# Kernel tuning notes

Hardware: AMD Instinct MI355X
Metric: run time of the kernel (lower is better)

The kernel has to match this reference:

```python
import jax, jax.numpy as jnp
import numpy as np

BN_EPS = 1e-5

def setup_inputs() -> dict:
    key = jax.random.key(0)
    B, C, T, N = 64, 1, 1024, 512
    weighted_fmri = jax.random.normal(key, (B, C, T, N), dtype=jnp.float32)
    bn_weight = jnp.ones((1,), dtype=jnp.float32)   # BatchNorm2d(1) affine weight
    bn_bias = jnp.zeros((1,), dtype=jnp.float32)    # BatchNorm2d(1) affine bias
    return {"weighted_fmri": weighted_fmri, "bn_weight": bn_weight, "bn_bias": bn_bias}


def reference(weighted_fmri, bn_weight, bn_bias):
    # weighted_fmri: [B, 1, T, N]. Original applies BatchNorm2d(1) per-sample
    # (batch of size 1 in training mode => normalize each sample by its own
    # mean/biased-var over (T, N)), then corrcoef over ROIs (columns).
    x = weighted_fmri
    mean = jnp.mean(x, axis=(1, 2, 3), keepdims=True)           # [B,1,1,1]
    var = jnp.mean((x - mean) ** 2, axis=(1, 2, 3), keepdims=True)  # biased var
    w = bn_weight.reshape(1, -1, 1, 1)
    b = bn_bias.reshape(1, -1, 1, 1)
    y = (x - mean) * jax.lax.rsqrt(var + BN_EPS) * w + b        # [B,1,T,N]

    X = y[:, 0]                                                 # [B,T,N]
    T = X.shape[1]
    # corrcoef(X.T): variables = N ROIs, observations = T timepoints
    Xc = X - jnp.mean(X, axis=1, keepdims=True)                 # center over time
    cov = jnp.einsum("btn,btm->bnm", Xc, Xc) / (T - 1)          # [B,N,N]
    d = jnp.sqrt(jnp.diagonal(cov, axis1=1, axis2=2))           # [B,N]
    corr = cov / (d[:, :, None] * d[:, None, :])
    return jnp.clip(corr, -1.0, 1.0)                            # [B,N,N]
```

## Files before the change

kernel.cpp:

```cpp
#include <hip/hip_runtime.h>

typedef __attribute__((ext_vector_type(8))) short bf16x8;
typedef __attribute__((ext_vector_type(4))) short s16x4;
typedef __attribute__((ext_vector_type(4))) float f32x4;

#define B_ 64
#define T_ 1024
#define N_ 512

__device__ __forceinline__ void async16(const void* g, void* l) {
  __builtin_amdgcn_global_load_lds(
      (const __attribute__((address_space(1))) unsigned int*)g,
      (__attribute__((address_space(3))) unsigned int*)l, 16, 0, 0);
}

__device__ __forceinline__ short f2bf(float f) {
  unsigned u = __builtin_bit_cast(unsigned, f);
  u += 0x7fffu + ((u >> 16) & 1u);
  return (short)(u >> 16);
}
__device__ __forceinline__ float bf2f(short s) {
  return __builtin_bit_cast(float, ((unsigned)(unsigned short)s) << 16);
}

__global__ __launch_bounds__(256, 4) void k_prep(
    const float* __restrict__ X, short* __restrict__ XbT,
    float* __restrict__ amu, float* __restrict__ invd)
{
  __shared__ __align__(16) short tile[64][68];
  const int b   = blockIdx.y;
  const int n0  = blockIdx.x * 64;
  const int tid = threadIdx.x;
  const int nch = tid & 15;
  const int rg  = tid >> 4;

  float s[4] = {0.f,0.f,0.f,0.f}, q[4] = {0.f,0.f,0.f,0.f};

  for (int tt = 0; tt < 16; ++tt) {
    const int t0 = tt * 64;
    #pragma unroll
    for (int i = 0; i < 4; ++i) {
      const int tr = rg + i * 16;
      const float4 v = *(const float4*)&X[((size_t)b*T_ + t0 + tr)*N_ + n0 + nch*4];
      short bb[4];
      bb[0] = f2bf(v.x); bb[1] = f2bf(v.y); bb[2] = f2bf(v.z); bb[3] = f2bf(v.w);
      #pragma unroll
      for (int c = 0; c < 4; ++c) { float f = bf2f(bb[c]); s[c] += f; q[c] += f*f; }
      s16x4 pk = { bb[0], bb[1], bb[2], bb[3] };
      *(s16x4*)&tile[tr][nch*4] = pk;
    }
    __syncthreads();
    #pragma unroll
    for (int i = 0; i < 4; ++i) {
      const int n = rg + i * 16;
      s16x4 o = { tile[nch*4+0][n], tile[nch*4+1][n],
                  tile[nch*4+2][n], tile[nch*4+3][n] };
      *(s16x4*)&XbT[((size_t)b*N_ + n0 + n)*T_ + t0 + nch*4] = o;
    }
    __syncthreads();
  }

  float* fb = (float*)&tile[0][0];
  #pragma unroll
  for (int c = 0; c < 4; ++c) { fb[tid*8 + c] = s[c]; fb[tid*8 + 4 + c] = q[c]; }
  __syncthreads();
  if (tid < 64) {
    const int qc = tid >> 2, c = tid & 3;
    float cs = 0.f, sq = 0.f;
    #pragma unroll
    for (int g = 0; g < 16; ++g) {
      cs += fb[(g*16 + qc)*8 + c];
      sq += fb[(g*16 + qc)*8 + 4 + c];
    }
    const int n = n0 + qc*4 + c;
    amu[b*N_ + n]  = cs * (1.f/32.f);
    invd[b*N_ + n] = rsqrtf(fmaxf(sq - cs*cs*(1.f/1024.f), 1e-20f));
  }
}

__global__ __launch_bounds__(256, 2) void k_gram(
    const short* __restrict__ XbT, const float* __restrict__ amu,
    const float* __restrict__ invd, float* __restrict__ out)
{
  __shared__ __align__(16) short ldsA[2][128][32];
  __shared__ __align__(16) short ldsB[2][128][32];

  const int bid = (blockIdx.x & 7) * 80 + (blockIdx.x >> 3);
  const int b = bid / 10;
  const int t = bid - b * 10;
  const int ip = (t >= 4) + (t >= 7) + (t >= 9);
  const int jp = ip + t - ((ip * (9 - ip)) >> 1);
  const int rowBase = ip * 128, colBase = jp * 128;
  const bool diag = (ip == jp);

  const int tid = threadIdx.x, lane = tid & 63, wave = tid >> 6;
  const int wr = wave >> 1, wc = wave & 1;
  const short* Xb = XbT + (size_t)b * N_ * T_;

  const int r0 = tid >> 2, cl = tid & 3;
  const int cg = cl ^ ((r0 >> 1) & 3);
  const size_t ga0 = (size_t)(rowBase + r0)      * T_ + cg * 8;
  const size_t ga1 = (size_t)(rowBase + r0 + 64) * T_ + cg * 8;
  const size_t gb0 = (size_t)(colBase + r0)      * T_ + cg * 8;
  const size_t gb1 = (size_t)(colBase + r0 + 64) * T_ + cg * 8;

  const int fr = lane & 15, kc = lane >> 4;
  const int swz = (kc ^ ((fr >> 1) & 3)) * 8;

  f32x4 acc[4][4] = {};

  #define STAGE(bufi, kb)                                                    \
    do {                                                                     \
      char* la_ = (char*)&ldsA[bufi][0][0];                                  \
      async16(Xb + ga0 + (kb), la_ + tid * 16);                              \
      async16(Xb + ga1 + (kb), la_ + (tid + 256) * 16);                      \
      if (!diag) {                                                           \
        char* lb_ = (char*)&ldsB[bufi][0][0];                                \
        async16(Xb + gb0 + (kb), lb_ + tid * 16);                            \
        async16(Xb + gb1 + (kb), lb_ + (tid + 256) * 16);                    \
      }                                                                      \
    } while (0)

  STAGE(0, 0);
  __syncthreads();
  int cur = 0;
  #pragma unroll 1
  for (int kt = 0; kt < 32; ++kt) {
    if (kt < 31) STAGE(cur ^ 1, (kt + 1) * 32);
    const short (*A)[32]  = ldsA[cur];
    const short (*Bm)[32] = diag ? ldsA[cur] : ldsB[cur];
    bf16x8 af[4], bfv[4];
    #pragma unroll
    for (int mi = 0; mi < 4; ++mi)
      af[mi] = *(const bf16x8*)&A[wr*64 + mi*16 + fr][swz];
    #pragma unroll
    for (int ni = 0; ni < 4; ++ni)
      bfv[ni] = *(const bf16x8*)&Bm[wc*64 + ni*16 + fr][swz];
    #pragma unroll
    for (int mi = 0; mi < 4; ++mi)
      #pragma unroll
      for (int ni = 0; ni < 4; ++ni)
        acc[mi][ni] = __builtin_amdgcn_mfma_f32_16x16x32_bf16(
            af[mi], bfv[ni], acc[mi][ni], 0, 0, 0);
    __syncthreads();
    cur ^= 1;
  }

  const int jc = colBase + wc * 64 + fr;
  float aj[4], dj[4];
  #pragma unroll
  for (int ni = 0; ni < 4; ++ni) {
    aj[ni] = amu[b*N_ + jc + ni*16];
    dj[ni] = invd[b*N_ + jc + ni*16];
  }
  #pragma unroll
  for (int mi = 0; mi < 4; ++mi) {
    const int ibase = rowBase + wr*64 + mi*16 + kc*4;
    float ai[4], di[4];
    #pragma unroll
    for (int r = 0; r < 4; ++r) {
      ai[r] = amu[b*N_ + ibase + r];
      di[r] = invd[b*N_ + ibase + r];
    }
    #pragma unroll
    for (int ni = 0; ni < 4; ++ni) {
      f32x4 g;
      #pragma unroll
      for (int r = 0; r < 4; ++r) {
        float v = (acc[mi][ni][r] - ai[r]*aj[ni]) * (di[r]*dj[ni]);
        g[r] = fminf(fmaxf(v, -1.f), 1.f);
      }
      const int J = jc + ni*16;
      #pragma unroll
      for (int r = 0; r < 4; ++r)
        out[((size_t)b*N_ + ibase + r)*N_ + J] = g[r];
      if (!diag)
        *(f32x4*)&out[((size_t)b*N_ + J)*N_ + ibase] = g;
    }
  }
}

extern "C" void kernel_launch(void* const* d_in, const int* in_sizes, int n_in,
                              void* d_out, int out_size, void* d_ws, size_t ws_size,
                              hipStream_t stream) {
  const float* X = (const float*)d_in[0];
  float* out = (float*)d_out;

  char* ws = (char*)d_ws;
  short* XbT  = (short*)ws;
  size_t off  = (size_t)B_ * N_ * T_ * sizeof(short);
  float* amu  = (float*)(ws + off);
  float* invd = amu + B_ * N_;

  k_prep<<<dim3(N_/64, B_), 256, 0, stream>>>(X, XbT, amu, invd);
  k_gram<<<dim3(64 * 10), 256, 0, stream>>>(XbT, amu, invd, out);
}
```

Before: 70.07 us.

## Fuse bf16 conversion into Gram kernels and compute stats via MFMA on diagonal tiles

```diff
diff --git a/kernel.cpp b/kernel.cpp
--- a/kernel.cpp
+++ b/kernel.cpp
@@ -1,4 +1,5 @@
 #include <hip/hip_runtime.h>
+#include <hip/hip_bf16.h>
 
 typedef __attribute__((ext_vector_type(8))) short bf16x8;
 typedef __attribute__((ext_vector_type(4))) short s16x4;
@@ -8,140 +9,171 @@
 #define T_ 1024
 #define N_ 512
 
-__device__ __forceinline__ void async16(const void* g, void* l) {
-  __builtin_amdgcn_global_load_lds(
-      (const __attribute__((address_space(1))) unsigned int*)g,
-      (__attribute__((address_space(3))) unsigned int*)l, 16, 0, 0);
-}
-
-__device__ __forceinline__ short f2bf(float f) {
-  unsigned u = __builtin_bit_cast(unsigned, f);
-  u += 0x7fffu + ((u >> 16) & 1u);
-  return (short)(u >> 16);
-}
-__device__ __forceinline__ float bf2f(short s) {
-  return __builtin_bit_cast(float, ((unsigned)(unsigned short)s) << 16);
-}
-
-__global__ __launch_bounds__(256, 4) void k_prep(
-    const float* __restrict__ X, short* __restrict__ XbT,
-    float* __restrict__ amu, float* __restrict__ invd)
+struct Slab { float4 v[4]; };
+
+__device__ __forceinline__ void slab_load(const float* __restrict__ Xb, int kb,
+                                          int pbase, int tid, Slab& s) {
+  const int n = (tid & 31) * 4, k = (tid >> 5) * 4;
+  const float* base = Xb + (size_t)(kb + k) * N_ + pbase + n;
+  #pragma unroll
+  for (int r = 0; r < 4; ++r)
+    s.v[r] = *(const float4*)(base + (size_t)r * N_);
+}
+
+__device__ __forceinline__ void slab_write(short* lds, int tid, const Slab& s) {
+  const int nq = tid & 31, kq = tid >> 5;
+  const int cg = kq >> 1, h = kq & 1;
+  const float* f = (const float*)&s.v[0];
+  #pragma unroll
+  for (int c = 0; c < 4; ++c) {
+    const int row = nq * 4 + c;
+    const int cc = cg ^ ((row >> 1) & 3);
+    s16x4 pk;
+    #pragma unroll
+    for (int r = 0; r < 4; ++r)
+      pk[r] = __builtin_bit_cast(short, __float2bfloat16(f[r * 4 + c]));
+    *(s16x4*)&lds[row * 32 + cc * 8 + h * 4] = pk;
+  }
+}
+
+__device__ __forceinline__ bf16x8 frag(const short* lds, int row, int kc) {
+  return *(const bf16x8*)&lds[row * 32 + ((kc ^ ((row >> 1) & 3)) * 8)];
+}
+
+__global__ __launch_bounds__(256, 2) void k_diag(
+    const float* __restrict__ X, float* __restrict__ amu,
+    float* __restrict__ invd, float* __restrict__ out)
 {
-  __shared__ __align__(16) short tile[64][68];
-  const int b   = blockIdx.y;
-  const int n0  = blockIdx.x * 64;
-  const int tid = threadIdx.x;
-  const int nch = tid & 15;
-  const int rg  = tid >> 4;
-
-  float s[4] = {0.f,0.f,0.f,0.f}, q[4] = {0.f,0.f,0.f,0.f};
-
-  for (int tt = 0; tt < 16; ++tt) {
-    const int t0 = tt * 64;
-    #pragma unroll
-    for (int i = 0; i < 4; ++i) {
-      const int tr = rg + i * 16;
-      const float4 v = *(const float4*)&X[((size_t)b*T_ + t0 + tr)*N_ + n0 + nch*4];
-      short bb[4];
-      bb[0] = f2bf(v.x); bb[1] = f2bf(v.y); bb[2] = f2bf(v.z); bb[3] = f2bf(v.w);
-      #pragma unroll
-      for (int c = 0; c < 4; ++c) { float f = bf2f(bb[c]); s[c] += f; q[c] += f*f; }
-      s16x4 pk = { bb[0], bb[1], bb[2], bb[3] };
-      *(s16x4*)&tile[tr][nch*4] = pk;
-    }
+  __shared__ __align__(16) short lds[2][128 * 32];
+  __shared__ float sAmu[128], sInvd[128];
+  const int p = blockIdx.x, b = blockIdx.y, pbase = p * 128;
+  const int tid = threadIdx.x, lane = tid & 63, wave = tid >> 6;
+  const int wr = wave >> 1, wc = wave & 1;
+  const int fr = lane & 15, kc = lane >> 4;
+  const float* Xb = X + (size_t)b * T_ * N_;
+
+  f32x4 acc[4][4] = {};
+  f32x4 accR[4] = {};
+  const short oneb = (short)0x3F80;
+  const bf16x8 ones = { oneb,oneb,oneb,oneb,oneb,oneb,oneb,oneb };
+
+  #define COMPUTE(BUF)                                                        \
+    do {                                                                      \
+      bf16x8 af[4], bfv[4];                                                   \
+      _Pragma("unroll")                                                       \
+      for (int mi = 0; mi < 4; ++mi) af[mi] = frag(BUF, wr*64 + mi*16 + fr, kc); \
+      _Pragma("unroll")                                                       \
+      for (int ni = 0; ni < 4; ++ni) bfv[ni] = frag(BUF, wc*64 + ni*16 + fr, kc); \
+      _Pragma("unroll")                                                       \
+      for (int mi = 0; mi < 4; ++mi) {                                        \
+        accR[mi] = __builtin_amdgcn_mfma_f32_16x16x32_bf16(af[mi], ones, accR[mi], 0,0,0); \
+        _Pragma("unroll")                                                     \
+        for (int ni = 0; ni < 4; ++ni)                                        \
+          acc[mi][ni] = __builtin_amdgcn_mfma_f32_16x16x32_bf16(af[mi], bfv[ni], acc[mi][ni], 0,0,0); \
+      }                                                                       \
+    } while (0)
+
+  Slab sA, sB;
+  slab_load(Xb, 0,  pbase, tid, sA);
+  slab_load(Xb, 32, pbase, tid, sB);
+  slab_write(lds[0], tid, sA);
+  __syncthreads();
+  #pragma unroll 1
+  for (int kt = 0; kt < 32; kt += 2) {
+    if (kt + 2 < 32) slab_load(Xb, (kt + 2) * 32, pbase, tid, sA);
+    COMPUTE(lds[0]);
+    slab_write(lds[1], tid, sB);
     __syncthreads();
-    #pragma unroll
-    for (int i = 0; i < 4; ++i) {
-      const int n = rg + i * 16;
-      s16x4 o = { tile[nch*4+0][n], tile[nch*4+1][n],
-                  tile[nch*4+2][n], tile[nch*4+3][n] };
-      *(s16x4*)&XbT[((size_t)b*N_ + n0 + n)*T_ + t0 + nch*4] = o;
-    }
+    if (kt + 3 < 32) slab_load(Xb, (kt + 3) * 32, pbase, tid, sB);
+    COMPUTE(lds[1]);
+    if (kt + 2 < 32) slab_write(lds[0], tid, sA);
     __syncthreads();
   }
 
-  float* fb = (float*)&tile[0][0];
-  #pragma unroll
-  for (int c = 0; c < 4; ++c) { fb[tid*8 + c] = s[c]; fb[tid*8 + 4 + c] = q[c]; }
+  if ((wave == 0 || wave == 3) && kc == (fr >> 2)) {
+    const int r = fr & 3;
+    #pragma unroll
+    for (int mi = 0; mi < 4; ++mi) {
+      const int il = wr * 64 + mi * 16 + fr;
+      const float rs  = accR[mi][r];
+      const float sii = acc[mi][mi][r];
+      const float a  = rs * (1.f / 32.f);
+      const float id = rsqrtf(fmaxf(sii - rs * rs * (1.f / 1024.f), 1e-20f));
+      sAmu[il] = a; sInvd[il] = id;
+      amu [b * N_ + pbase + il] = a;
+      invd[b * N_ + pbase + il] = id;
+    }
+  }
   __syncthreads();
-  if (tid < 64) {
-    const int qc = tid >> 2, c = tid & 3;
-    float cs = 0.f, sq = 0.f;
-    #pragma unroll
-    for (int g = 0; g < 16; ++g) {
-      cs += fb[(g*16 + qc)*8 + c];
-      sq += fb[(g*16 + qc)*8 + 4 + c];
-    }
-    const int n = n0 + qc*4 + c;
-    amu[b*N_ + n]  = cs * (1.f/32.f);
-    invd[b*N_ + n] = rsqrtf(fmaxf(sq - cs*cs*(1.f/1024.f), 1e-20f));
-  }
-}
-
-__global__ __launch_bounds__(256, 2) void k_gram(
-    const short* __restrict__ XbT, const float* __restrict__ amu,
+
+  const int jl = wc * 64 + fr;
+  float aj[4], dj[4];
+  #pragma unroll
+  for (int ni = 0; ni < 4; ++ni) { aj[ni] = sAmu[jl + ni*16]; dj[ni] = sInvd[jl + ni*16]; }
+  #pragma unroll
+  for (int mi = 0; mi < 4; ++mi) {
+    const int il = wr * 64 + mi * 16 + kc * 4;
+    float ai[4], di[4];
+    #pragma unroll
+    for (int r = 0; r < 4; ++r) { ai[r] = sAmu[il + r]; di[r] = sInvd[il + r]; }
+    #pragma unroll
+    for (int ni = 0; ni < 4; ++ni) {
+      #pragma unroll
+      for (int r = 0; r < 4; ++r) {
+        float v = (acc[mi][ni][r] - ai[r] * aj[ni]) * (di[r] * dj[ni]);
+        v = fminf(fmaxf(v, -1.f), 1.f);
+        out[((size_t)b * N_ + pbase + il + r) * N_ + pbase + jl + ni * 16] = v;
+      }
+    }
+  }
+  #undef COMPUTE
+}
+
+__global__ __launch_bounds__(256, 2) void k_off(
+    const float* __restrict__ X, const float* __restrict__ amu,
     const float* __restrict__ invd, float* __restrict__ out)
 {
-  __shared__ __align__(16) short ldsA[2][128][32];
-  __shared__ __align__(16) short ldsB[2][128][32];
-
-  const int bid = (blockIdx.x & 7) * 80 + (blockIdx.x >> 3);
-  const int b = bid / 10;
-  const int t = bid - b * 10;
-  const int ip = (t >= 4) + (t >= 7) + (t >= 9);
-  const int jp = ip + t - ((ip * (9 - ip)) >> 1);
+  __shared__ __align__(16) short ldsA[2][128 * 32];
+  __shared__ __align__(16) short ldsB[2][128 * 32];
+  const int bid = (blockIdx.x & 7) * 48 + (blockIdx.x >> 3);
+  const int b = bid / 6, t = bid - b * 6;
+  const int ip = (t >= 3) + (t >= 5);
+  const int jp = (ip == 0) ? t + 1 : (ip == 1 ? t - 1 : 3);
   const int rowBase = ip * 128, colBase = jp * 128;
-  const bool diag = (ip == jp);
-
   const int tid = threadIdx.x, lane = tid & 63, wave = tid >> 6;
   const int wr = wave >> 1, wc = wave & 1;
-  const short* Xb = XbT + (size_t)b * N_ * T_;
-
-  const int r0 = tid >> 2, cl = tid & 3;
-  const int cg = cl ^ ((r0 >> 1) & 3);
-  const size_t ga0 = (size_t)(rowBase + r0)      * T_ + cg * 8;
-  const size_t ga1 = (size_t)(rowBase + r0 + 64) * T_ + cg * 8;
-  const size_t gb0 = (size_t)(colBase + r0)      * T_ + cg * 8;
-  const size_t gb1 = (size_t)(colBase + r0 + 64) * T_ + cg * 8;
-
   const int fr = lane & 15, kc = lane >> 4;
-  const int swz = (kc ^ ((fr >> 1) & 3)) * 8;
+  const float* Xb = X + (size_t)b * T_ * N_;
 
   f32x4 acc[4][4] = {};
 
-  #define STAGE(bufi, kb)                                                    \
-    do {                                                                     \
-      char* la_ = (char*)&ldsA[bufi][0][0];                                  \
-      async16(Xb + ga0 + (kb), la_ + tid * 16);                              \
-      async16(Xb + ga1 + (kb), la_ + (tid + 256) * 16);                      \
-      if (!diag) {                                                           \
-        char* lb_ = (char*)&ldsB[bufi][0][0];                                \
-        async16(Xb + gb0 + (kb), lb_ + tid * 16);                            \
-        async16(Xb + gb1 + (kb), lb_ + (tid + 256) * 16);                    \
-      }                                                                      \
-    } while (0)
-
-  STAGE(0, 0);
+  Slab a0, b0;
+  slab_load(Xb, 0, rowBase, tid, a0);
+  slab_load(Xb, 0, colBase, tid, b0);
+  slab_write(ldsA[0], tid, a0);
+  slab_write(ldsB[0], tid, b0);
   __syncthreads();
   int cur = 0;
   #pragma unroll 1
   for (int kt = 0; kt < 32; ++kt) {
-    if (kt < 31) STAGE(cur ^ 1, (kt + 1) * 32);
-    const short (*A)[32]  = ldsA[cur];
-    const short (*Bm)[32] = diag ? ldsA[cur] : ldsB[cur];
+    if (kt < 31) {
+      slab_load(Xb, (kt + 1) * 32, rowBase, tid, a0);
+      slab_load(Xb, (kt + 1) * 32, colBase, tid, b0);
+    }
     bf16x8 af[4], bfv[4];
     #pragma unroll
+    for (int mi = 0; mi < 4; ++mi) af[mi] = frag(ldsA[cur], wr*64 + mi*16 + fr, kc);
+    #pragma unroll
+    for (int ni = 0; ni < 4; ++ni) bfv[ni] = frag(ldsB[cur], wc*64 + ni*16 + fr, kc);
+    #pragma unroll
     for (int mi = 0; mi < 4; ++mi)
-      af[mi] = *(const bf16x8*)&A[wr*64 + mi*16 + fr][swz];
-    #pragma unroll
-    for (int ni = 0; ni < 4; ++ni)
-      bfv[ni] = *(const bf16x8*)&Bm[wc*64 + ni*16 + fr][swz];
-    #pragma unroll
-    for (int mi = 0; mi < 4; ++mi)
       #pragma unroll
       for (int ni = 0; ni < 4; ++ni)
-        acc[mi][ni] = __builtin_amdgcn_mfma_f32_16x16x32_bf16(
-            af[mi], bfv[ni], acc[mi][ni], 0, 0, 0);
+        acc[mi][ni] = __builtin_amdgcn_mfma_f32_16x16x32_bf16(af[mi], bfv[ni], acc[mi][ni], 0,0,0);
+    if (kt < 31) {
+      slab_write(ldsA[cur ^ 1], tid, a0);
+      slab_write(ldsB[cur ^ 1], tid, b0);
+    }
     __syncthreads();
     cur ^= 1;
   }
@@ -150,32 +182,31 @@
   float aj[4], dj[4];
   #pragma unroll
   for (int ni = 0; ni < 4; ++ni) {
-    aj[ni] = amu[b*N_ + jc + ni*16];
-    dj[ni] = invd[b*N_ + jc + ni*16];
+    aj[ni] = amu [b * N_ + jc + ni * 16];
+    dj[ni] = invd[b * N_ + jc + ni * 16];
   }
   #pragma unroll
   for (int mi = 0; mi < 4; ++mi) {
-    const int ibase = rowBase + wr*64 + mi*16 + kc*4;
+    const int ibase = rowBase + wr * 64 + mi * 16 + kc * 4;
     float ai[4], di[4];
     #pragma unroll
     for (int r = 0; r < 4; ++r) {
-      ai[r] = amu[b*N_ + ibase + r];
-      di[r] = invd[b*N_ + ibase + r];
+      ai[r] = amu [b * N_ + ibase + r];
+      di[r] = invd[b * N_ + ibase + r];
     }
     #pragma unroll
     for (int ni = 0; ni < 4; ++ni) {
       f32x4 g;
       #pragma unroll
       for (int r = 0; r < 4; ++r) {
-        float v = (acc[mi][ni][r] - ai[r]*aj[ni]) * (di[r]*dj[ni]);
+        float v = (acc[mi][ni][r] - ai[r] * aj[ni]) * (di[r] * dj[ni]);
         g[r] = fminf(fmaxf(v, -1.f), 1.f);
       }
-      const int J = jc + ni*16;
+      const int J = jc + ni * 16;
       #pragma unroll
       for (int r = 0; r < 4; ++r)
-        out[((size_t)b*N_ + ibase + r)*N_ + J] = g[r];
-      if (!diag)
-        *(f32x4*)&out[((size_t)b*N_ + J)*N_ + ibase] = g;
+        out[((size_t)b * N_ + ibase + r) * N_ + J] = g[r];
+      *(f32x4*)&out[((size_t)b * N_ + J) * N_ + ibase] = g;
     }
   }
 }
@@ -186,12 +217,9 @@
   const float* X = (const float*)d_in[0];
   float* out = (float*)d_out;
 
-  char* ws = (char*)d_ws;
-  short* XbT  = (short*)ws;
-  size_t off  = (size_t)B_ * N_ * T_ * sizeof(short);
-  float* amu  = (float*)(ws + off);
+  float* amu  = (float*)d_ws;
   float* invd = amu + B_ * N_;
 
-  k_prep<<<dim3(N_/64, B_), 256, 0, stream>>>(X, XbT, amu, invd);
-  k_gram<<<dim3(64 * 10), 256, 0, stream>>>(XbT, amu, invd, out);
-}
+  k_diag<<<dim3(4, B_), 256, 0, stream>>>(X, amu, invd, out);
+  k_off<<<dim3(8 * 48), 256, 0, stream>>>(X, amu, invd, out);
+}
```

After: 76.21 us. 1.09x slower.

## Triple-buffer gram kernel LDS pipeline with explicit vmcnt waits and diag specialization

Applied to the files above, without the earlier changes.

```diff
diff --git a/kernel.cpp b/kernel.cpp
--- a/kernel.cpp
+++ b/kernel.cpp
@@ -1,4 +1,5 @@
 #include <hip/hip_runtime.h>
+#include <hip/hip_bf16.h>
 
 typedef __attribute__((ext_vector_type(8))) short bf16x8;
 typedef __attribute__((ext_vector_type(4))) short s16x4;
@@ -7,6 +8,10 @@
 #define B_ 64
 #define T_ 1024
 #define N_ 512
+
+#define FENCE() asm volatile("" ::: "memory")
+#define VMWAIT(N) asm volatile("s_waitcnt vmcnt(" #N ")" ::: "memory")
+#define BAR() __builtin_amdgcn_s_barrier()
 
 __device__ __forceinline__ void async16(const void* g, void* l) {
   __builtin_amdgcn_global_load_lds(
@@ -15,9 +20,7 @@
 }
 
 __device__ __forceinline__ short f2bf(float f) {
-  unsigned u = __builtin_bit_cast(unsigned, f);
-  u += 0x7fffu + ((u >> 16) & 1u);
-  return (short)(u >> 16);
+  return __builtin_bit_cast(short, __float2bfloat16(f));
 }
 __device__ __forceinline__ float bf2f(short s) {
   return __builtin_bit_cast(float, ((unsigned)(unsigned short)s) << 16);
@@ -78,12 +81,78 @@
   }
 }
 
-__global__ __launch_bounds__(256, 2) void k_gram(
+__device__ __forceinline__ void compute_step(
+    const short* A, const short* Bm, int aoff, int boff, int swz,
+    f32x4 (&acc)[4][4])
+{
+  bf16x8 af[4], bfv[4];
+  #pragma unroll
+  for (int mi = 0; mi < 4; ++mi) af[mi] = *(const bf16x8*)&A[aoff + mi*512 + swz];
+  #pragma unroll
+  for (int ni = 0; ni < 4; ++ni) bfv[ni] = *(const bf16x8*)&Bm[boff + ni*512 + swz];
+  #pragma unroll
+  for (int mi = 0; mi < 4; ++mi)
+    #pragma unroll
+    for (int ni = 0; ni < 4; ++ni)
+      acc[mi][ni] = __builtin_amdgcn_mfma_f32_16x16x32_bf16(
+          af[mi], bfv[ni], acc[mi][ni], 0, 0, 0);
+}
+
+template<bool DIAG>
+__device__ __forceinline__ void gram_main(
+    const short* __restrict__ Xb,
+    size_t ga0, size_t ga1, size_t gb0, size_t gb1,
+    short (*ldsA)[4096], short (*ldsB)[4096],
+    int tid, int aoff, int boff, int swz, f32x4 (&acc)[4][4])
+{
+  auto stg = [&](int bi, int kb) {
+    char* la = (char*)ldsA[bi];
+    async16(Xb + ga0 + kb, la + tid*16);
+    async16(Xb + ga1 + kb, la + (tid+256)*16);
+    if (!DIAG) {
+      char* lb = (char*)ldsB[bi];
+      async16(Xb + gb0 + kb, lb + tid*16);
+      async16(Xb + gb1 + kb, lb + (tid+256)*16);
+    }
+  };
+  auto cmp = [&](int bi) {
+    compute_step(ldsA[bi], DIAG ? ldsA[bi] : ldsB[bi], aoff, boff, swz, acc);
+  };
+
+  stg(0, 0); stg(1, 32);
+  #pragma unroll 1
+  for (int it = 0; it < 10; ++it) {
+    stg(2, (3*it + 2) * 32);
+    if (DIAG) { VMWAIT(4); } else { VMWAIT(8); }
+    BAR(); FENCE();
+    cmp(0);
+    FENCE(); BAR();
+    stg(0, (3*it + 3) * 32);
+    if (DIAG) { VMWAIT(4); } else { VMWAIT(8); }
+    BAR(); FENCE();
+    cmp(1);
+    FENCE(); BAR();
+    stg(1, (3*it + 4) * 32);
+    if (DIAG) { VMWAIT(4); } else { VMWAIT(8); }
+    BAR(); FENCE();
+    cmp(2);
+    FENCE(); BAR();
+  }
+  if (DIAG) { VMWAIT(2); } else { VMWAIT(4); }
+  BAR(); FENCE();
+  cmp(0);
+  FENCE(); BAR();
+  VMWAIT(0);
+  BAR(); FENCE();
+  cmp(1);
+}
+
+__global__ __launch_bounds__(256, 3) void k_gram(
     const short* __restrict__ XbT, const float* __restrict__ amu,
     const float* __restrict__ invd, float* __restrict__ out)
 {
-  __shared__ __align__(16) short ldsA[2][128][32];
-  __shared__ __align__(16) short ldsB[2][128][32];
+  __shared__ __align__(16) short ldsA[3][4096];
+  __shared__ __align__(16) short ldsB[3][4096];
 
   const int bid = (blockIdx.x & 7) * 80 + (blockIdx.x >> 3);
   const int b = bid / 10;
@@ -105,52 +174,19 @@
   const size_t gb1 = (size_t)(colBase + r0 + 64) * T_ + cg * 8;
 
   const int fr = lane & 15, kc = lane >> 4;
-  const int swz = (kc ^ ((fr >> 1) & 3)) * 8;
+  const int swz  = (kc ^ ((fr >> 1) & 3)) * 8;
+  const int aoff = (wr * 64 + fr) * 32;
+  const int boff = (wc * 64 + fr) * 32;
 
   f32x4 acc[4][4] = {};
-
-  #define STAGE(bufi, kb)                                                    \
-    do {                                                                     \
-      char* la_ = (char*)&ldsA[bufi][0][0];                                  \
-      async16(Xb + ga0 + (kb), la_ + tid * 16);                              \
-      async16(Xb + ga1 + (kb), la_ + (tid + 256) * 16);                      \
-      if (!diag) {                                                           \
-        char* lb_ = (char*)&ldsB[bufi][0][0];                                \
-        async16(Xb + gb0 + (kb), lb_ + tid * 16);                            \
-        async16(Xb + gb1 + (kb), lb_ + (tid + 256) * 16);                    \
-      }                                                                      \
-    } while (0)
-
-  STAGE(0, 0);
-  __syncthreads();
-  int cur = 0;
-  #pragma unroll 1
-  for (int kt = 0; kt < 32; ++kt) {
-    if (kt < 31) STAGE(cur ^ 1, (kt + 1) * 32);
-    const short (*A)[32]  = ldsA[cur];
-    const short (*Bm)[32] = diag ? ldsA[cur] : ldsB[cur];
-    bf16x8 af[4], bfv[4];
-    #pragma unroll
-    for (int mi = 0; mi < 4; ++mi)
-      af[mi] = *(const bf16x8*)&A[wr*64 + mi*16 + fr][swz];
-    #pragma unroll
-    for (int ni = 0; ni < 4; ++ni)
-      bfv[ni] = *(const bf16x8*)&Bm[wc*64 + ni*16 + fr][swz];
-    #pragma unroll
-    for (int mi = 0; mi < 4; ++mi)
-      #pragma unroll
-      for (int ni = 0; ni < 4; ++ni)
-        acc[mi][ni] = __builtin_amdgcn_mfma_f32_16x16x32_bf16(
-            af[mi], bfv[ni], acc[mi][ni], 0, 0, 0);
-    __syncthreads();
-    cur ^= 1;
-  }
+  if (diag) gram_main<true >(Xb, ga0, ga1, gb0, gb1, ldsA, ldsB, tid, aoff, boff, swz, acc);
+  else      gram_main<false>(Xb, ga0, ga1, gb0, gb1, ldsA, ldsB, tid, aoff, boff, swz, acc);
 
   const int jc = colBase + wc * 64 + fr;
   float aj[4], dj[4];
   #pragma unroll
   for (int ni = 0; ni < 4; ++ni) {
-    aj[ni] = amu[b*N_ + jc + ni*16];
+    aj[ni] = amu [b*N_ + jc + ni*16];
     dj[ni] = invd[b*N_ + jc + ni*16];
   }
   #pragma unroll
@@ -159,7 +195,7 @@
     float ai[4], di[4];
     #pragma unroll
     for (int r = 0; r < 4; ++r) {
-      ai[r] = amu[b*N_ + ibase + r];
+      ai[r] = amu [b*N_ + ibase + r];
       di[r] = invd[b*N_ + ibase + r];
     }
     #pragma unroll
@@ -170,7 +206,7 @@
         float v = (acc[mi][ni][r] - ai[r]*aj[ni]) * (di[r]*dj[ni]);
         g[r] = fminf(fmaxf(v, -1.f), 1.f);
       }
-      const int J = jc + ni*16;
+      const int J = jc + ni * 16;
       #pragma unroll
       for (int r = 0; r < 4; ++r)
         out[((size_t)b*N_ + ibase + r)*N_ + J] = g[r];
```

Result: faster. 68.24 us (-2.6%).

## Fuse bf16 transpose-prep into gram kernel, computing column stats in-block

Applied to the files above, without the earlier changes.

```diff
diff --git a/kernel.cpp b/kernel.cpp
--- a/kernel.cpp
+++ b/kernel.cpp
@@ -1,4 +1,5 @@
 #include <hip/hip_runtime.h>
+#include <hip/hip_bf16.h>
 
 typedef __attribute__((ext_vector_type(8))) short bf16x8;
 typedef __attribute__((ext_vector_type(4))) short s16x4;
@@ -8,82 +9,66 @@
 #define T_ 1024
 #define N_ 512
 
-__device__ __forceinline__ void async16(const void* g, void* l) {
-  __builtin_amdgcn_global_load_lds(
-      (const __attribute__((address_space(1))) unsigned int*)g,
-      (__attribute__((address_space(3))) unsigned int*)l, 16, 0, 0);
-}
-
 __device__ __forceinline__ short f2bf(float f) {
-  unsigned u = __builtin_bit_cast(unsigned, f);
-  u += 0x7fffu + ((u >> 16) & 1u);
-  return (short)(u >> 16);
+  return __builtin_bit_cast(short, __float2bfloat16(f));
 }
 __device__ __forceinline__ float bf2f(short s) {
   return __builtin_bit_cast(float, ((unsigned)(unsigned short)s) << 16);
 }
 
-__global__ __launch_bounds__(256, 4) void k_prep(
-    const float* __restrict__ X, short* __restrict__ XbT,
-    float* __restrict__ amu, float* __restrict__ invd)
-{
-  __shared__ __align__(16) short tile[64][68];
-  const int b   = blockIdx.y;
-  const int n0  = blockIdx.x * 64;
-  const int tid = threadIdx.x;
-  const int nch = tid & 15;
-  const int rg  = tid >> 4;
+struct Slab { float4 v[4]; };
 
-  float s[4] = {0.f,0.f,0.f,0.f}, q[4] = {0.f,0.f,0.f,0.f};
+__device__ __forceinline__ void slab_load(const float* __restrict__ Xb, int kb,
+                                          int pbase, int tid, Slab& s) {
+  const int n = (tid & 31) * 4, k = (tid >> 5) * 4;
+  const float* base = Xb + (size_t)(kb + k) * N_ + pbase + n;
+  #pragma unroll
+  for (int r = 0; r < 4; ++r)
+    s.v[r] = *(const float4*)(base + (size_t)r * N_);
+}
 
-  for (int tt = 0; tt < 16; ++tt) {
-    const int t0 = tt * 64;
+__device__ __forceinline__ void slab_write(short* lds, int tid, const Slab& s,
+                                           float (&st)[4], float (&qt)[4]) {
+  const int nq = tid & 31, kq = tid >> 5;
+  const int cg = kq >> 1, h = kq & 1;
+  const float* f = (const float*)&s.v[0];
+  #pragma unroll
+  for (int c = 0; c < 4; ++c) {
+    const int row = nq * 4 + c;
+    const int cc = cg ^ ((row >> 1) & 3);
+    s16x4 pk;
     #pragma unroll
-    for (int i = 0; i < 4; ++i) {
-      const int tr = rg + i * 16;
-      const float4 v = *(const float4*)&X[((size_t)b*T_ + t0 + tr)*N_ + n0 + nch*4];
-      short bb[4];
-      bb[0] = f2bf(v.x); bb[1] = f2bf(v.y); bb[2] = f2bf(v.z); bb[3] = f2bf(v.w);
-      #pragma unroll
-      for (int c = 0; c < 4; ++c) { float f = bf2f(bb[c]); s[c] += f; q[c] += f*f; }
-      s16x4 pk = { bb[0], bb[1], bb[2], bb[3] };
-      *(s16x4*)&tile[tr][nch*4] = pk;
+    for (int r = 0; r < 4; ++r) {
+      pk[r] = f2bf(f[r * 4 + c]);
+      const float fv = bf2f(pk[r]);
+      st[c] += fv; qt[c] += fv * fv;
     }
-    __syncthreads();
-    #pragma unroll
-    for (int i = 0; i < 4; ++i) {
-      const int n = rg + i * 16;
-      s16x4 o = { tile[nch*4+0][n], tile[nch*4+1][n],
-                  tile[nch*4+2][n], tile[nch*4+3][n] };
-      *(s16x4*)&XbT[((size_t)b*N_ + n0 + n)*T_ + t0 + nch*4] = o;
-    }
-    __syncthreads();
-  }
-
-  float* fb = (float*)&tile[0][0];
-  #pragma unroll
-  for (int c = 0; c < 4; ++c) { fb[tid*8 + c] = s[c]; fb[tid*8 + 4 + c] = q[c]; }
-  __syncthreads();
-  if (tid < 64) {
-    const int qc = tid >> 2, c = tid & 3;
-    float cs = 0.f, sq = 0.f;
-    #pragma unroll
-    for (int g = 0; g < 16; ++g) {
-      cs += fb[(g*16 + qc)*8 + c];
-      sq += fb[(g*16 + qc)*8 + 4 + c];
-    }
-    const int n = n0 + qc*4 + c;
-    amu[b*N_ + n]  = cs * (1.f/32.f);
-    invd[b*N_ + n] = rsqrtf(fmaxf(sq - cs*cs*(1.f/1024.f), 1e-20f));
+    *(s16x4*)&lds[row * 32 + cc * 8 + h * 4] = pk;
   }
 }
 
-__global__ __launch_bounds__(256, 2) void k_gram(
-    const short* __restrict__ XbT, const float* __restrict__ amu,
-    const float* __restrict__ invd, float* __restrict__ out)
+__device__ __forceinline__ void compute_step(
+    const short* A, const short* Bm, int aoff, int boff, int swz,
+    f32x4 (&acc)[4][4])
 {
-  __shared__ __align__(16) short ldsA[2][128][32];
-  __shared__ __align__(16) short ldsB[2][128][32];
+  bf16x8 af[4], bfv[4];
+  #pragma unroll
+  for (int mi = 0; mi < 4; ++mi) af[mi] = *(const bf16x8*)&A[aoff + mi*512 + swz];
+  #pragma unroll
+  for (int ni = 0; ni < 4; ++ni) bfv[ni] = *(const bf16x8*)&Bm[boff + ni*512 + swz];
+  #pragma unroll
+  for (int mi = 0; mi < 4; ++mi)
+    #pragma unroll
+    for (int ni = 0; ni < 4; ++ni)
+      acc[mi][ni] = __builtin_amdgcn_mfma_f32_16x16x32_bf16(
+          af[mi], bfv[ni], acc[mi][ni], 0, 0, 0);
+}
+
+__global__ __launch_bounds__(256, 3) void k_fused(
+    const float* __restrict__ X, float* __restrict__ out)
+{
+  __shared__ __align__(16) short lds[2][2][4096];
+  __shared__ float sMu[256], sId[256];
 
   const int bid = (blockIdx.x & 7) * 80 + (blockIdx.x >> 3);
   const int b = bid / 10;
@@ -95,87 +80,93 @@
 
   const int tid = threadIdx.x, lane = tid & 63, wave = tid >> 6;
   const int wr = wave >> 1, wc = wave & 1;
-  const short* Xb = XbT + (size_t)b * N_ * T_;
+  const int fr = lane & 15, kc = lane >> 4;
+  const int swz  = (kc ^ ((fr >> 1) & 3)) * 8;
+  const int aoff = (wr * 64 + fr) * 32;
+  const int boff = (wc * 64 + fr) * 32;
+  const float* Xb = X + (size_t)b * T_ * N_;
 
-  const int r0 = tid >> 2, cl = tid & 3;
-  const int cg = cl ^ ((r0 >> 1) & 3);
-  const size_t ga0 = (size_t)(rowBase + r0)      * T_ + cg * 8;
-  const size_t ga1 = (size_t)(rowBase + r0 + 64) * T_ + cg * 8;
-  const size_t gb0 = (size_t)(colBase + r0)      * T_ + cg * 8;
-  const size_t gb1 = (size_t)(colBase + r0 + 64) * T_ + cg * 8;
-
-  const int fr = lane & 15, kc = lane >> 4;
-  const int swz = (kc ^ ((fr >> 1) & 3)) * 8;
-
+  float sA[4] = {0,0,0,0}, qA[4] = {0,0,0,0};
+  float sB[4] = {0,0,0,0}, qB[4] = {0,0,0,0};
   f32x4 acc[4][4] = {};
 
-  #define STAGE(bufi, kb)                                                    \
-    do {                                                                     \
-      char* la_ = (char*)&ldsA[bufi][0][0];                                  \
-      async16(Xb + ga0 + (kb), la_ + tid * 16);                              \
-      async16(Xb + ga1 + (kb), la_ + (tid + 256) * 16);                      \
-      if (!diag) {                                                           \
-        char* lb_ = (char*)&ldsB[bufi][0][0];                                \
-        async16(Xb + gb0 + (kb), lb_ + tid * 16);                            \
-        async16(Xb + gb1 + (kb), lb_ + (tid + 256) * 16);                    \
-      }                                                                      \
-    } while (0)
+  Slab a, bb;
+  slab_load(Xb, 0, rowBase, tid, a);
+  if (!diag) slab_load(Xb, 0, colBase, tid, bb);
+  slab_write(lds[0][0], tid, a, sA, qA);
+  if (!diag) slab_write(lds[0][1], tid, bb, sB, qB);
+  __syncthreads();
 
-  STAGE(0, 0);
-  __syncthreads();
   int cur = 0;
   #pragma unroll 1
   for (int kt = 0; kt < 32; ++kt) {
-    if (kt < 31) STAGE(cur ^ 1, (kt + 1) * 32);
-    const short (*A)[32]  = ldsA[cur];
-    const short (*Bm)[32] = diag ? ldsA[cur] : ldsB[cur];
-    bf16x8 af[4], bfv[4];
-    #pragma unroll
-    for (int mi = 0; mi < 4; ++mi)
-      af[mi] = *(const bf16x8*)&A[wr*64 + mi*16 + fr][swz];
-    #pragma unroll
-    for (int ni = 0; ni < 4; ++ni)
-      bfv[ni] = *(const bf16x8*)&Bm[wc*64 + ni*16 + fr][swz];
-    #pragma unroll
-    for (int mi = 0; mi < 4; ++mi)
-      #pragma unroll
-      for (int ni = 0; ni < 4; ++ni)
-        acc[mi][ni] = __builtin_amdgcn_mfma_f32_16x16x32_bf16(
-            af[mi], bfv[ni], acc[mi][ni], 0, 0, 0);
+    if (kt < 31) {
+      slab_load(Xb, (kt + 1) * 32, rowBase, tid, a);
+      if (!diag) slab_load(Xb, (kt + 1) * 32, colBase, tid, bb);
+    }
+    compute_step(lds[cur][0], diag ? lds[cur][0] : lds[cur][1],
+                 aoff, boff, swz, acc);
+    if (kt < 31) {
+      slab_write(lds[cur ^ 1][0], tid, a, sA, qA);
+      if (!diag) slab_write(lds[cur ^ 1][1], tid, bb, sB, qB);
+    }
     __syncthreads();
     cur ^= 1;
   }
 
-  const int jc = colBase + wc * 64 + fr;
+  float* fb = (float*)&lds[0][0][0];
+  const int nq = tid & 31, kq = tid >> 5;
+  #pragma unroll
+  for (int c = 0; c < 4; ++c) {
+    const int col = nq * 4 + c;
+    fb[       col * 8 + kq] = sA[c];
+    fb[1024 + col * 8 + kq] = qA[c];
+    fb[2048 + col * 8 + kq] = sB[c];
+    fb[3072 + col * 8 + kq] = qB[c];
+  }
+  __syncthreads();
+  {
+    const int base = (tid < 128) ? 0 : 2048;
+    const int col  = tid & 127;
+    float rs = 0.f, ss = 0.f;
+    #pragma unroll
+    for (int k = 0; k < 8; ++k) {
+      rs += fb[base +        col * 8 + k];
+      ss += fb[base + 1024 + col * 8 + k];
+    }
+    sMu[tid] = rs * (1.f / 32.f);
+    sId[tid] = rsqrtf(fmaxf(ss - rs * rs * (1.f / 1024.f), 1e-20f));
+  }
+  __syncthreads();
+
+  const int jb = diag ? 0 : 128;
+  const int jl = wc * 64 + fr;
   float aj[4], dj[4];
   #pragma unroll
   for (int ni = 0; ni < 4; ++ni) {
-    aj[ni] = amu[b*N_ + jc + ni*16];
-    dj[ni] = invd[b*N_ + jc + ni*16];
+    aj[ni] = sMu[jb + jl + ni * 16];
+    dj[ni] = sId[jb + jl + ni * 16];
   }
   #pragma unroll
   for (int mi = 0; mi < 4; ++mi) {
-    const int ibase = rowBase + wr*64 + mi*16 + kc*4;
+    const int il = wr * 64 + mi * 16 + kc * 4;
     float ai[4], di[4];
     #pragma unroll
-    for (int r = 0; r < 4; ++r) {
-      ai[r] = amu[b*N_ + ibase + r];
-      di[r] = invd[b*N_ + ibase + r];
-    }
+    for (int r = 0; r < 4; ++r) { ai[r] = sMu[il + r]; di[r] = sId[il + r]; }
     #pragma unroll
     for (int ni = 0; ni < 4; ++ni) {
       f32x4 g;
       #pragma unroll
       for (int r = 0; r < 4; ++r) {
-        float v = (acc[mi][ni][r] - ai[r]*aj[ni]) * (di[r]*dj[ni]);
+        float v = (acc[mi][ni][r] - ai[r] * aj[ni]) * (di[r] * dj[ni]);
         g[r] = fminf(fmaxf(v, -1.f), 1.f);
       }
-      const int J = jc + ni*16;
+      const int J = colBase + jl + ni * 16;
       #pragma unroll
       for (int r = 0; r < 4; ++r)
-        out[((size_t)b*N_ + ibase + r)*N_ + J] = g[r];
+        out[((size_t)b * N_ + rowBase + il + r) * N_ + J] = g[r];
       if (!diag)
-        *(f32x4*)&out[((size_t)b*N_ + J)*N_ + ibase] = g;
+        *(f32x4*)&out[((size_t)b * N_ + J) * N_ + rowBase + il] = g;
     }
   }
 }
@@ -185,13 +176,5 @@
                               hipStream_t stream) {
   const float* X = (const float*)d_in[0];
   float* out = (float*)d_out;
-
-  char* ws = (char*)d_ws;
-  short* XbT  = (short*)ws;
-  size_t off  = (size_t)B_ * N_ * T_ * sizeof(short);
-  float* amu  = (float*)(ws + off);
-  float* invd = amu + B_ * N_;
-
-  k_prep<<<dim3(N_/64, B_), 256, 0, stream>>>(X, XbT, amu, invd);
-  k_gram<<<dim3(64 * 10), 256, 0, stream>>>(XbT, amu, invd, out);
+  k_fused<<<dim3(640), 256, 0, stream>>>(X, out);
 }
```

Measured after the change: 88.22 us. 1.26x slower.
